# Kernel optimization log

Measured on AMD Instinct MI355X. Metric: run time of the kernel, lower is better.

The kernel has to match this reference:

```python
import jax, jax.numpy as jnp
import numpy as np

B, W, D = 8, 1024, 1024
HEADS, KDIM, VDIM = 16, 64, 64


def setup_inputs() -> dict:
    key = jax.random.key(0)
    k1, k2, k3, k4 = jax.random.split(key, 4)
    # he_normal-ish scaling for weights
    s = (2.0 / D) ** 0.5
    return {
        "inputs": jax.random.normal(k1, (B, W, D), dtype=jnp.float32),
        "Wq": jax.random.normal(k2, (D, HEADS * KDIM), dtype=jnp.float32) * s,
        "Wk": jax.random.normal(k3, (D, HEADS * KDIM), dtype=jnp.float32) * s,
        "Wv": jax.random.normal(k4, (D, HEADS * VDIM), dtype=jnp.float32) * s,
    }


def reference(inputs, Wq, Wk, Wv):
    # Self-attention: memory = inputs
    bsz, win, _ = inputs.shape
    # DenseHeads: linear projection, reshaped to (B, W, heads, head_units)
    q = (inputs @ Wq).reshape(bsz, win, HEADS, KDIM)
    k = (inputs @ Wk).reshape(bsz, win, HEADS, KDIM)
    v = (inputs @ Wv).reshape(bsz, win, HEADS, VDIM)
    scale = KDIM ** (-0.5)
    # scores[b,q,h,m] = sum_k Q[b,q,h,k] * K[b,m,h,k]
    scores = jnp.einsum("bqhk,bmhk->bqhm", q, k) * scale
    attn = jax.nn.softmax(scores, axis=-1)
    # out[b,q,h,v] = sum_m attn[b,q,h,m] * V[b,m,h,v]
    out = jnp.einsum("bqhm,bmhv->bqhv", attn, v)
    return out
```

## Files before the change

### kernel.cpp

```cpp
#include <hip/hip_runtime.h>
#include <stdint.h>


using bf16x8 = __attribute__((ext_vector_type(8))) __bf16;
using f32x4  = __attribute__((ext_vector_type(4))) float;
using f16x4  = __attribute__((ext_vector_type(4))) _Float16;

union frag_u  { uint4 u4; bf16x8 f; };
union vfrag_u { uint2 u2; f16x4 f; };
union pfrag_u { unsigned int u[2]; f16x4 f; };

__device__ inline unsigned short f2bf(float x){
  unsigned int u = __float_as_uint(x);
  u += 0x7fffu + ((u >> 16) & 1u);
  return (unsigned short)(u >> 16);
}

__device__ inline unsigned int pkrtz_u32(float a, float b){
  auto r = __builtin_amdgcn_cvt_pkrtz(a, b);
  unsigned int u; __builtin_memcpy(&u, &r, 4); return u;
}

__device__ inline void gl_lds16(const void* g, void* l){
  __builtin_amdgcn_global_load_lds(
      (const __attribute__((address_space(1))) void*)g,
      (__attribute__((address_space(3))) void*)l, 16, 0, 0);
}

__global__ void cast_x(const float* __restrict__ X, unsigned short* __restrict__ Xb){
  int i = (blockIdx.x * 256 + threadIdx.x) * 4;
  float4 v = *(const float4*)(X + i);
  ushort4 o;
  o.x = f2bf(v.x); o.y = f2bf(v.y); o.z = f2bf(v.z); o.w = f2bf(v.w);
  *(ushort4*)(Xb + i) = o;
}

__global__ void cast_wt(const float* __restrict__ Wq, const float* __restrict__ Wk,
                        const float* __restrict__ Wv, unsigned short* __restrict__ Wt){
  __shared__ float tile[64][65];
  int id = blockIdx.x;
  int proj = id >> 8;
  int rem  = id & 255;
  int kt = rem & 15, nt = rem >> 4;
  const float* Wsrc = (proj == 0) ? Wq : ((proj == 1) ? Wk : Wv);
  int k0 = kt * 64, n0 = nt * 64;
  int tx = threadIdx.x & 63, ty = threadIdx.x >> 6;
  for (int i = 0; i < 16; i++){
    int k = i * 4 + ty;
    tile[k][tx] = Wsrc[(k0 + k) * 1024 + n0 + tx];
  }
  __syncthreads();
  for (int i = 0; i < 16; i++){
    int n = i * 4 + ty;
    Wt[(proj * 1024 + n0 + n) * 1024 + k0 + tx] = f2bf(tile[tx][n]);
  }
}

__global__ void gemm_qkv(const unsigned short* __restrict__ Xb,
                         const unsigned short* __restrict__ Wt,
                         unsigned short* __restrict__ QK,
                         unsigned short* __restrict__ Vt){
  __shared__ __align__(16) unsigned short Abuf[128 * 64];
  __shared__ __align__(16) unsigned short Bbuf[128 * 64];
  int bid = blockIdx.x;
  int bx = bid % 24, by = bid / 24;
  int w = threadIdx.x >> 6, lane = threadIdx.x & 63;
  int g = lane >> 4, li = lane & 15;
  int lrow = lane >> 3, lcol = lane & 7;
  int wm = (w >> 1) * 64, wn = (w & 1) * 64;
  f32x4 acc[4][4] = {};

  for (int k0 = 0; k0 < 1024; k0 += 64){
    __syncthreads();
    for (int i = 0; i < 4; i++){
      int idx = w * 4 + i;
      int row = idx * 8 + lrow;
      gl_lds16(Xb + (by * 128 + row) * 1024 + k0 + lcol * 8, Abuf + idx * 512);
      gl_lds16(Wt + (bx * 128 + row) * 1024 + k0 + lcol * 8, Bbuf + idx * 512);
    }
    __syncthreads();
    for (int c = 0; c < 2; c++){
      frag_u a[4], b[4];
      for (int i = 0; i < 4; i++)
        a[i].u4 = *(const uint4*)(Abuf + (wm + i * 16 + li) * 64 + c * 32 + g * 8);
      for (int j = 0; j < 4; j++)
        b[j].u4 = *(const uint4*)(Bbuf + (wn + j * 16 + li) * 64 + c * 32 + g * 8);
      for (int i = 0; i < 4; i++)
        for (int j = 0; j < 4; j++)
          acc[i][j] = __builtin_amdgcn_mfma_f32_16x16x32_bf16(a[i].f, b[j].f, acc[i][j], 0, 0, 0);
    }
  }
  if (bx >= 16){
    for (int i = 0; i < 4; i++){
      int row = by * 128 + wm + i * 16 + g * 4;
      int bb = row >> 10, m = row & 1023;
      for (int j = 0; j < 4; j++){
        int vc = bx * 128 + wn + j * 16 + li - 2048;
        int hh = vc >> 6, dd = vc & 63;
        uint2 cv;
        cv.x = pkrtz_u32(acc[i][j][0], acc[i][j][1]);
        cv.y = pkrtz_u32(acc[i][j][2], acc[i][j][3]);
        *(uint2*)(Vt + ((size_t)(bb * 16 + hh) * 64 + dd) * 1024 + m) = cv;
      }
    }
  } else {
    float sc = (bx < 8) ? 0.1803368801111f : 1.0f;
    for (int i = 0; i < 4; i++){
      int row = by * 128 + wm + i * 16 + g * 4;
      for (int j = 0; j < 4; j++){
        int col = bx * 128 + wn + j * 16 + li;
        for (int r = 0; r < 4; r++)
          QK[(size_t)(row + r) * 2048 + col] = f2bf(acc[i][j][r] * sc);
      }
    }
  }
}

__global__ __launch_bounds__(256) void attn(const unsigned short* __restrict__ QK,
                                            const unsigned short* __restrict__ Vt,
                                            float* __restrict__ Out){
  __shared__ __align__(16) unsigned short Kbuf[64 * 64];
  __shared__ __align__(16) unsigned short Vbuf[64 * 64];
  int id = blockIdx.x;
  int bh = id & 127, qb = id >> 7;
  int b = bh >> 4, h = bh & 15;
  int w = threadIdx.x >> 6, lane = threadIdx.x & 63;
  int g = lane >> 4, li = lane & 15;
  int lrow = lane >> 3, lcol = lane & 7;
  int scol = ((lcol ^ lrow) & 7) * 8;

  frag_u qf[2][2];
  for (int u = 0; u < 2; u++){
    int tok = b * 1024 + qb * 128 + w * 32 + u * 16 + li;
    const unsigned short* qp = QK + (size_t)tok * 2048 + h * 64 + g * 8;
    qf[u][0].u4 = *(const uint4*)(qp);
    qf[u][1].u4 = *(const uint4*)(qp + 32);
  }

  f32x4 o[2][4] = {};
  float psum[2] = {0.f, 0.f};
  const f32x4 bias = {-10.f, -10.f, -10.f, -10.f};

  const unsigned short* Kg = QK + (size_t)b * 1024 * 2048 + 1024 + h * 64;
  const unsigned short* Vg = Vt + (size_t)bh * 65536;

  for (int mt = 0; mt < 16; mt++){
    int m0 = mt * 64;
    __syncthreads();
    for (int i = 0; i < 2; i++){
      int idx = w * 2 + i;
      int row = idx * 8 + lrow;
      gl_lds16(Kg + (size_t)(m0 + row) * 2048 + scol, Kbuf + idx * 512);
      gl_lds16(Vg + row * 1024 + m0 + scol, Vbuf + idx * 512);
    }
    __syncthreads();

    f32x4 s[2][4];
    for (int u = 0; u < 2; u++)
      for (int t = 0; t < 4; t++)
        s[u][t] = bias;
    for (int t = 0; t < 4; t++){
      for (int c = 0; c < 2; c++){
        frag_u kf;
        kf.u4 = *(const uint4*)(Kbuf + (t * 16 + li) * 64 + ((((c << 2) + g) ^ (li & 7)) << 3));
        s[0][t] = __builtin_amdgcn_mfma_f32_16x16x32_bf16(kf.f, qf[0][c].f, s[0][t], 0, 0, 0);
        s[1][t] = __builtin_amdgcn_mfma_f32_16x16x32_bf16(kf.f, qf[1][c].f, s[1][t], 0, 0, 0);
      }
    }

    pfrag_u pf[2][4];
    for (int u = 0; u < 2; u++){
      for (int t = 0; t < 4; t++){
        float p0 = __builtin_exp2f(s[u][t][0]);
        float p1 = __builtin_exp2f(s[u][t][1]);
        float p2 = __builtin_exp2f(s[u][t][2]);
        float p3 = __builtin_exp2f(s[u][t][3]);
        psum[u] += (p0 + p1) + (p2 + p3);
        pf[u][t].u[0] = pkrtz_u32(p0, p1);
        pf[u][t].u[1] = pkrtz_u32(p2, p3);
      }
    }

    for (int tv = 0; tv < 4; tv++){
      for (int t = 0; t < 4; t++){
        int gg = ((t * 2 + (g >> 1)) ^ (li & 7));
        vfrag_u vf;
        vf.u2 = *(const uint2*)(Vbuf + (tv * 16 + li) * 64 + gg * 8 + (g & 1) * 4);
        o[0][tv] = __builtin_amdgcn_mfma_f32_16x16x16f16(vf.f, pf[0][t].f, o[0][tv], 0, 0, 0);
        o[1][tv] = __builtin_amdgcn_mfma_f32_16x16x16f16(vf.f, pf[1][t].f, o[1][tv], 0, 0, 0);
      }
    }
  }

  for (int u = 0; u < 2; u++){
    psum[u] += __shfl_xor(psum[u], 16);
    psum[u] += __shfl_xor(psum[u], 32);
  }

  for (int u = 0; u < 2; u++){
    float inv = 1.f / psum[u];
    int tok = b * 1024 + qb * 128 + w * 32 + u * 16 + li;
    float* op = Out + (size_t)tok * 1024 + h * 64 + g * 4;
    for (int tv = 0; tv < 4; tv++){
      float4 v4;
      v4.x = o[u][tv][0] * inv; v4.y = o[u][tv][1] * inv;
      v4.z = o[u][tv][2] * inv; v4.w = o[u][tv][3] * inv;
      *(float4*)(op + tv * 16) = v4;
    }
  }
}

extern "C" void kernel_launch(void* const* d_in, const int* in_sizes, int n_in,
                              void* d_out, int out_size, void* d_ws, size_t ws_size,
                              hipStream_t stream) {
  const float* X  = (const float*)d_in[0];
  const float* Wq = (const float*)d_in[1];
  const float* Wk = (const float*)d_in[2];
  const float* Wv = (const float*)d_in[3];
  float* Out = (float*)d_out;
  char* ws = (char*)d_ws;
  unsigned short* Xb = (unsigned short*)(ws);
  unsigned short* Wt = (unsigned short*)(ws + (size_t)16 * 1024 * 1024);
  unsigned short* QK = (unsigned short*)(ws + (size_t)22 * 1024 * 1024);
  unsigned short* Vt = (unsigned short*)(ws + (size_t)54 * 1024 * 1024);

  cast_x  <<<8192, 256, 0, stream>>>(X, Xb);
  cast_wt <<<768,  256, 0, stream>>>(Wq, Wk, Wv, Wt);
  gemm_qkv<<<1536, 256, 0, stream>>>(Xb, Wt, QK, Vt);
  attn    <<<1024, 256, 0, stream>>>(QK, Vt, Out);
}
```

Baseline: 221.6 us.

## Merge cast kernels, remap GEMM block order, halve attention query tile

The two cast kernels become one launch, with block ID used to dispatch between the X cast and the weight transpose-cast. The QKV GEMM block mapping changes so that consecutive blocks share the same weight column tile (by varies fastest), which should improve L2 reuse of Wt. The attention kernel now handles 64 queries per block instead of 128, doubling the grid to 2048 blocks and cutting register pressure for more parallelism. The cost is that each K/V tile loaded into LDS is reused by half as many queries, so K/V traffic doubles.

```diff
diff --git a/kernel.cpp b/kernel.cpp
--- a/kernel.cpp
+++ b/kernel.cpp
@@ -27,18 +27,22 @@
       (__attribute__((address_space(3))) void*)l, 16, 0, 0);
 }
 
-__global__ void cast_x(const float* __restrict__ X, unsigned short* __restrict__ Xb){
-  int i = (blockIdx.x * 256 + threadIdx.x) * 4;
-  float4 v = *(const float4*)(X + i);
-  ushort4 o;
-  o.x = f2bf(v.x); o.y = f2bf(v.y); o.z = f2bf(v.z); o.w = f2bf(v.w);
-  *(ushort4*)(Xb + i) = o;
-}
-
-__global__ void cast_wt(const float* __restrict__ Wq, const float* __restrict__ Wk,
-                        const float* __restrict__ Wv, unsigned short* __restrict__ Wt){
+__global__ void cast_all(const float* __restrict__ X,
+                         const float* __restrict__ Wq, const float* __restrict__ Wk,
+                         const float* __restrict__ Wv,
+                         unsigned short* __restrict__ Xb,
+                         unsigned short* __restrict__ Wt){
   __shared__ float tile[64][65];
-  int id = blockIdx.x;
+  int bid = blockIdx.x;
+  if (bid < 8192){
+    int i = (bid * 256 + threadIdx.x) * 4;
+    float4 v = *(const float4*)(X + i);
+    ushort4 o;
+    o.x = f2bf(v.x); o.y = f2bf(v.y); o.z = f2bf(v.z); o.w = f2bf(v.w);
+    *(ushort4*)(Xb + i) = o;
+    return;
+  }
+  int id = bid - 8192;
   int proj = id >> 8;
   int rem  = id & 255;
   int kt = rem & 15, nt = rem >> 4;
@@ -63,7 +67,7 @@
   __shared__ __align__(16) unsigned short Abuf[128 * 64];
   __shared__ __align__(16) unsigned short Bbuf[128 * 64];
   int bid = blockIdx.x;
-  int bx = bid % 24, by = bid / 24;
+  int bx = bid >> 6, by = bid & 63;
   int w = threadIdx.x >> 6, lane = threadIdx.x & 63;
   int g = lane >> 4, li = lane & 15;
   int lrow = lane >> 3, lcol = lane & 7;
@@ -129,16 +133,16 @@
   int lrow = lane >> 3, lcol = lane & 7;
   int scol = ((lcol ^ lrow) & 7) * 8;
 
-  frag_u qf[2][2];
-  for (int u = 0; u < 2; u++){
-    int tok = b * 1024 + qb * 128 + w * 32 + u * 16 + li;
+  frag_u qf[2];
+  {
+    int tok = b * 1024 + qb * 64 + w * 16 + li;
     const unsigned short* qp = QK + (size_t)tok * 2048 + h * 64 + g * 8;
-    qf[u][0].u4 = *(const uint4*)(qp);
-    qf[u][1].u4 = *(const uint4*)(qp + 32);
-  }
-
-  f32x4 o[2][4] = {};
-  float psum[2] = {0.f, 0.f};
+    qf[0].u4 = *(const uint4*)(qp);
+    qf[1].u4 = *(const uint4*)(qp + 32);
+  }
+
+  f32x4 o[4] = {};
+  float psum = 0.f;
   const f32x4 bias = {-10.f, -10.f, -10.f, -10.f};
 
   const unsigned short* Kg = QK + (size_t)b * 1024 * 2048 + 1024 + h * 64;
@@ -151,34 +155,29 @@
       int idx = w * 2 + i;
       int row = idx * 8 + lrow;
       gl_lds16(Kg + (size_t)(m0 + row) * 2048 + scol, Kbuf + idx * 512);
-      gl_lds16(Vg + row * 1024 + m0 + scol, Vbuf + idx * 512);
-    }
-    __syncthreads();
-
-    f32x4 s[2][4];
-    for (int u = 0; u < 2; u++)
-      for (int t = 0; t < 4; t++)
-        s[u][t] = bias;
+      gl_lds16(Vg + row * 1024 + m0 + scol,           Vbuf + idx * 512);
+    }
+    __syncthreads();
+
+    f32x4 s[4];
+    for (int t = 0; t < 4; t++) s[t] = bias;
     for (int t = 0; t < 4; t++){
       for (int c = 0; c < 2; c++){
         frag_u kf;
         kf.u4 = *(const uint4*)(Kbuf + (t * 16 + li) * 64 + ((((c << 2) + g) ^ (li & 7)) << 3));
-        s[0][t] = __builtin_amdgcn_mfma_f32_16x16x32_bf16(kf.f, qf[0][c].f, s[0][t], 0, 0, 0);
-        s[1][t] = __builtin_amdgcn_mfma_f32_16x16x32_bf16(kf.f, qf[1][c].f, s[1][t], 0, 0, 0);
-      }
-    }
-
-    pfrag_u pf[2][4];
-    for (int u = 0; u < 2; u++){
-      for (int t = 0; t < 4; t++){
-        float p0 = __builtin_exp2f(s[u][t][0]);
-        float p1 = __builtin_exp2f(s[u][t][1]);
-        float p2 = __builtin_exp2f(s[u][t][2]);
-        float p3 = __builtin_exp2f(s[u][t][3]);
-        psum[u] += (p0 + p1) + (p2 + p3);
-        pf[u][t].u[0] = pkrtz_u32(p0, p1);
-        pf[u][t].u[1] = pkrtz_u32(p2, p3);
-      }
+        s[t] = __builtin_amdgcn_mfma_f32_16x16x32_bf16(kf.f, qf[c].f, s[t], 0, 0, 0);
+      }
+    }
+
+    pfrag_u pf[4];
+    for (int t = 0; t < 4; t++){
+      float p0 = __builtin_exp2f(s[t][0]);
+      float p1 = __builtin_exp2f(s[t][1]);
+      float p2 = __builtin_exp2f(s[t][2]);
+      float p3 = __builtin_exp2f(s[t][3]);
+      psum += (p0 + p1) + (p2 + p3);
+      pf[t].u[0] = pkrtz_u32(p0, p1);
+      pf[t].u[1] = pkrtz_u32(p2, p3);
     }
 
     for (int tv = 0; tv < 4; tv++){
@@ -186,27 +185,22 @@
         int gg = ((t * 2 + (g >> 1)) ^ (li & 7));
         vfrag_u vf;
         vf.u2 = *(const uint2*)(Vbuf + (tv * 16 + li) * 64 + gg * 8 + (g & 1) * 4);
-        o[0][tv] = __builtin_amdgcn_mfma_f32_16x16x16f16(vf.f, pf[0][t].f, o[0][tv], 0, 0, 0);
-        o[1][tv] = __builtin_amdgcn_mfma_f32_16x16x16f16(vf.f, pf[1][t].f, o[1][tv], 0, 0, 0);
-      }
-    }
-  }
-
-  for (int u = 0; u < 2; u++){
-    psum[u] += __shfl_xor(psum[u], 16);
-    psum[u] += __shfl_xor(psum[u], 32);
-  }
-
-  for (int u = 0; u < 2; u++){
-    float inv = 1.f / psum[u];
-    int tok = b * 1024 + qb * 128 + w * 32 + u * 16 + li;
-    float* op = Out + (size_t)tok * 1024 + h * 64 + g * 4;
-    for (int tv = 0; tv < 4; tv++){
-      float4 v4;
-      v4.x = o[u][tv][0] * inv; v4.y = o[u][tv][1] * inv;
-      v4.z = o[u][tv][2] * inv; v4.w = o[u][tv][3] * inv;
-      *(float4*)(op + tv * 16) = v4;
-    }
+        o[tv] = __builtin_amdgcn_mfma_f32_16x16x16f16(vf.f, pf[t].f, o[tv], 0, 0, 0);
+      }
+    }
+  }
+
+  psum += __shfl_xor(psum, 16);
+  psum += __shfl_xor(psum, 32);
+  float inv = 1.f / psum;
+
+  int tok = b * 1024 + qb * 64 + w * 16 + li;
+  float* op = Out + (size_t)tok * 1024 + h * 64 + g * 4;
+  for (int tv = 0; tv < 4; tv++){
+    float4 v4;
+    v4.x = o[tv][0] * inv; v4.y = o[tv][1] * inv;
+    v4.z = o[tv][2] * inv; v4.w = o[tv][3] * inv;
+    *(float4*)(op + tv * 16) = v4;
   }
 }
 
@@ -224,8 +218,7 @@
   unsigned short* QK = (unsigned short*)(ws + (size_t)22 * 1024 * 1024);
   unsigned short* Vt = (unsigned short*)(ws + (size_t)54 * 1024 * 1024);
 
-  cast_x  <<<8192, 256, 0, stream>>>(X, Xb);
-  cast_wt <<<768,  256, 0, stream>>>(Wq, Wk, Wv, Wt);
+  cast_all<<<8960, 256, 0, stream>>>(X, Wq, Wk, Wv, Xb, Wt);
   gemm_qkv<<<1536, 256, 0, stream>>>(Xb, Wt, QK, Vt);
-  attn    <<<1024, 256, 0, stream>>>(QK, Vt, Out);
-}
+  attn    <<<2048, 256, 0, stream>>>(QK, Vt, Out);
+}
```

Result: faster. 217.2 us (-2.0%).
